# Kernel tuning notes

Measured on AMD Instinct MI355X. Metric: run time of the kernel, lower is better.

Reference implementation:

```python
import jax, jax.numpy as jnp
import numpy as np

N_NODES = 100000
N_EDGES = 1600000


def _sage_layer(x, src, dst, Wl, bl, Wr):
    # PyG SAGEConv (aggr='mean', root_weight=True):
    #   out_i = lin_l(mean_{j in N(i)} x_j) + lin_r(x_i)
    msg = x[src]                                              # [E, d] gather
    summed = jax.ops.segment_sum(msg, dst, num_segments=N_NODES)
    cnt = jax.ops.segment_sum(jnp.ones((src.shape[0],), x.dtype), dst,
                              num_segments=N_NODES)
    mean = summed / jnp.maximum(cnt, 1.0)[:, None]            # zero-deg nodes -> 0
    return mean @ Wl + bl + x @ Wr


def setup_inputs() -> dict:
    key = jax.random.key(0)
    ks = jax.random.split(key, 12)
    d_in, d_h, d_out = 6, 128, 64

    def lin(k, fi, fo):
        s = 1.0 / np.sqrt(fi)
        return jax.random.uniform(k, (fi, fo), jnp.float32, -s, s)

    return {
        "x": jax.random.normal(ks[0], (N_NODES, 10), jnp.float32),
        "edge_index": jax.random.randint(ks[1], (2, N_EDGES), 0, N_NODES),
        "Wl0": lin(ks[2], d_in, d_h), "bl0": jnp.zeros((d_h,), jnp.float32),
        "Wr0": lin(ks[3], d_in, d_h),
        "Wl1": lin(ks[4], d_h, d_h), "bl1": jnp.zeros((d_h,), jnp.float32),
        "Wr1": lin(ks[5], d_h, d_h),
        "Wl2": lin(ks[6], d_h, d_out), "bl2": jnp.zeros((d_out,), jnp.float32),
        "Wr2": lin(ks[7], d_h, d_out),
    }


def reference(x, edge_index, Wl0, bl0, Wr0, Wl1, bl1, Wr1, Wl2, bl2, Wr2):
    src, dst = edge_index[0], edge_index[1]
    h = x[:, 4:10]                                            # bus feature slice
    h = jax.nn.relu(_sage_layer(h, src, dst, Wl0, bl0, Wr0))
    h = jax.nn.relu(_sage_layer(h, src, dst, Wl1, bl1, Wr1))
    h = jax.nn.relu(_sage_layer(h, src, dst, Wl2, bl2, Wr2))
    return h
```

## Files before the change

### kernel.cpp

```cpp
#include <hip/hip_runtime.h>


typedef __attribute__((ext_vector_type(8))) short bf16x8;
typedef __attribute__((ext_vector_type(4))) float f32x4;
typedef __attribute__((ext_vector_type(2))) float f32x2;

constexpr int PB = 256;
constexpr float F8SCALE = 32.0f;

static __device__ __forceinline__ int imax(int a, int b) { return a > b ? a : b; }

static __device__ __forceinline__ float bfbits_lo(unsigned u) {
    union { unsigned i; float f; } v; v.i = u << 16; return v.f;
}
static __device__ __forceinline__ float bfbits_hi(unsigned u) {
    union { unsigned i; float f; } v; v.i = u & 0xffff0000u; return v.f;
}
static __device__ __forceinline__ unsigned short f2bf(float f) {
    unsigned u = __float_as_uint(f);
    u = (u + 0x7fffu + ((u >> 16) & 1u)) >> 16;
    return (unsigned short)u;
}
static __device__ __forceinline__ unsigned pack2bf(float a, float b) {
    return (unsigned)f2bf(a) | ((unsigned)f2bf(b) << 16);
}
static __device__ __forceinline__ void acc_f8x4(unsigned u, float* a) {
    f32x2 lo = __builtin_amdgcn_cvt_pk_f32_fp8((int)u, false);
    f32x2 hi = __builtin_amdgcn_cvt_pk_f32_fp8((int)u, true);
    a[0] += lo[0]; a[1] += lo[1]; a[2] += hi[0]; a[3] += hi[1];
}
static __device__ __forceinline__ void acc_bf8(uint4 v, float* a) {
    a[0] += bfbits_lo(v.x); a[1] += bfbits_hi(v.x);
    a[2] += bfbits_lo(v.y); a[3] += bfbits_hi(v.y);
    a[4] += bfbits_lo(v.z); a[5] += bfbits_hi(v.z);
    a[6] += bfbits_lo(v.w); a[7] += bfbits_hi(v.w);
}


__global__ __launch_bounds__(256) void k_p1count(const int* __restrict__ dst,
                                                 int* __restrict__ C,
                                                 int nE, int nbk, int epb) {
    __shared__ int h[512];
    for (int i = threadIdx.x; i < nbk; i += 256) h[i] = 0;
    __syncthreads();
    int e0 = blockIdx.x * epb;
    int e1 = min(e0 + epb, nE);
    for (int i = e0 + threadIdx.x; i < e1; i += 256)
        atomicAdd(&h[dst[i] >> 8], 1);
    __syncthreads();
    for (int i = threadIdx.x; i < nbk; i += 256)
        C[blockIdx.x * nbk + i] = h[i];
}

__global__ __launch_bounds__(256) void k_colscan(int* __restrict__ C,
                                                 int* __restrict__ tot, int nbk) {
    __shared__ int sm[256];
    int k = blockIdx.x, t = threadIdx.x;
    int v = C[t * nbk + k];
    sm[t] = v;
    __syncthreads();
    for (int o = 1; o < 256; o <<= 1) {
        int u = (t >= o) ? sm[t - o] : 0;
        __syncthreads();
        sm[t] += u;
        __syncthreads();
    }
    C[t * nbk + k] = sm[t] - v;
    if (t == 255) tot[k] = sm[255];
}

__global__ __launch_bounds__(256) void k_scan_a(const int* __restrict__ cnt,
                                                int* __restrict__ offs, int n) {
    __shared__ int sm[256];
    int t = threadIdx.x;
    int base = t * 4;
    int v0 = 0, v1 = 0, v2 = 0, v3 = 0;
    if (base + 3 < n) {
        int4 q = *(const int4*)(cnt + base);
        v0 = q.x; v1 = q.y; v2 = q.z; v3 = q.w;
    } else {
        if (base < n)     v0 = cnt[base];
        if (base + 1 < n) v1 = cnt[base + 1];
        if (base + 2 < n) v2 = cnt[base + 2];
    }
    int s = v0 + v1 + v2 + v3;
    sm[t] = s;
    __syncthreads();
    for (int o = 1; o < 256; o <<= 1) {
        int u = (t >= o) ? sm[t - o] : 0;
        __syncthreads();
        sm[t] += u;
        __syncthreads();
    }
    int excl = sm[t] - s;
    if (base < n)     offs[base]     = excl;
    if (base + 1 < n) offs[base + 1] = excl + v0;
    if (base + 2 < n) offs[base + 2] = excl + v0 + v1;
    if (base + 3 < n) offs[base + 3] = excl + v0 + v1 + v2;
    if (t == 255) offs[n] = sm[255];
}

__global__ __launch_bounds__(256) void k_p1fill(const int* __restrict__ src,
                                                const int* __restrict__ dst,
                                                const int* __restrict__ bstart,
                                                const int* __restrict__ C,
                                                unsigned* __restrict__ ebuf,
                                                int nE, int nbk, int epb) {
    __shared__ int cur[512];
    int b = blockIdx.x;
    for (int i = threadIdx.x; i < nbk; i += 256)
        cur[i] = bstart[i] + C[b * nbk + i];
    __syncthreads();
    int e0 = b * epb;
    int e1 = min(e0 + epb, nE);
    for (int i = e0 + threadIdx.x; i < e1; i += 256) {
        int d = dst[i];
        unsigned s = (unsigned)src[i];
        int p = atomicAdd(&cur[d >> 8], 1);
        ebuf[p] = (s << 8) | (unsigned)(d & 255);
    }
}

__global__ __launch_bounds__(256) void k_p2fill(const unsigned* __restrict__ ebuf,
                                                const int* __restrict__ bstart,
                                                int* __restrict__ offs,
                                                int* __restrict__ csr,
                                                int nN, int nE) {
    __shared__ int h[256], sm[256], cur[256];
    int k = blockIdx.x, t = threadIdx.x;
    int base = bstart[k], end = bstart[k + 1];
    h[t] = 0;
    __syncthreads();
    for (int i = base + t; i < end; i += 256)
        atomicAdd(&h[ebuf[i] & 255u], 1);
    __syncthreads();
    int v = h[t];
    sm[t] = v;
    __syncthreads();
    for (int o = 1; o < 256; o <<= 1) {
        int u = (t >= o) ? sm[t - o] : 0;
        __syncthreads();
        sm[t] += u;
        __syncthreads();
    }
    int excl = sm[t] - v;
    int node = (k << 8) + t;
    if (node < nN) offs[node] = base + excl;
    cur[t] = base + excl;
    if (k == 0 && t == 0) offs[nN] = nE;
    __syncthreads();
    for (int i = base + t; i < end; i += 256) {
        unsigned e = ebuf[i];
        int p = atomicAdd(&cur[e & 255u], 1);
        csr[p] = (int)(e >> 8);
    }
}


static __device__ __forceinline__ void wtfrag_one(const float* __restrict__ W1,
                                                  const float* __restrict__ W2,
                                                  unsigned short* __restrict__ Wt,
                                                  int K1, int K, int N, int c) {
    int NB = N >> 4;
    int lane = c & 63;
    int n = (c >> 6) % NB;
    int ks = c / (NB << 6);
    int row = n * 16 + (lane & 15);
    int col = ks * 32 + (lane >> 4) * 8;
    unsigned short o[8];
#pragma unroll
    for (int j = 0; j < 8; ++j) {
        int k = col + j;
        float v = (k < K1) ? W1[k * N + row] : W2[(k - K1) * N + row];
        o[j] = f2bf(v);
    }
    *(uint4*)(Wt + (size_t)c * 8) = *(const uint4*)o;
}

__global__ __launch_bounds__(256) void k_wtfrag_all(const float* __restrict__ Wl1,
                                                    const float* __restrict__ Wr1,
                                                    const float* __restrict__ Wl2,
                                                    const float* __restrict__ Wr2,
                                                    unsigned short* __restrict__ Wt1,
                                                    unsigned short* __restrict__ Wt2l,
                                                    unsigned short* __restrict__ Wt2r) {
    int c = blockIdx.x * 256 + threadIdx.x;
    if (c < 4096)      wtfrag_one(Wl1, Wr1, Wt1, 128, 256, 128, c);
    else if (c < 5120) wtfrag_one(Wl2, Wl2, Wt2l, 128, 128, 64, c - 4096);
    else if (c < 6144) wtfrag_one(Wr2, Wr2, Wt2r, 128, 128, 64, c - 5120);
}


__global__ __launch_bounds__(256) void k_agg0(const float* __restrict__ x,
                                              const int* __restrict__ offs,
                                              const int* __restrict__ csr,
                                              float* __restrict__ mean0, int nN) {
    int i = blockIdx.x * blockDim.x + threadIdx.x;
    if (i >= nN) return;
    int lo = offs[i], hi = offs[i + 1];
    float a0 = 0, a1 = 0, a2 = 0, a3 = 0, a4 = 0, a5 = 0;
    int e = lo;
    for (; e + 4 <= hi; e += 4) {
        int s0 = csr[e], s1 = csr[e + 1], s2 = csr[e + 2], s3 = csr[e + 3];
        const float* r0 = x + (size_t)s0 * 10 + 4;
        const float* r1 = x + (size_t)s1 * 10 + 4;
        const float* r2 = x + (size_t)s2 * 10 + 4;
        const float* r3 = x + (size_t)s3 * 10 + 4;
        float2 u0 = *(const float2*)(r0), u1 = *(const float2*)(r0 + 2), u2 = *(const float2*)(r0 + 4);
        float2 w0 = *(const float2*)(r1), w1 = *(const float2*)(r1 + 2), w2 = *(const float2*)(r1 + 4);
        float2 p0 = *(const float2*)(r2), p1 = *(const float2*)(r2 + 2), p2 = *(const float2*)(r2 + 4);
        float2 q0 = *(const float2*)(r3), q1 = *(const float2*)(r3 + 2), q2 = *(const float2*)(r3 + 4);
        a0 += u0.x + w0.x + p0.x + q0.x;
        a1 += u0.y + w0.y + p0.y + q0.y;
        a2 += u1.x + w1.x + p1.x + q1.x;
        a3 += u1.y + w1.y + p1.y + q1.y;
        a4 += u2.x + w2.x + p2.x + q2.x;
        a5 += u2.y + w2.y + p2.y + q2.y;
    }
    for (; e < hi; ++e) {
        int s = csr[e];
        const float* r = x + (size_t)s * 10 + 4;
        float2 v0 = *(const float2*)(r);
        float2 v1 = *(const float2*)(r + 2);
        float2 v2 = *(const float2*)(r + 4);
        a0 += v0.x; a1 += v0.y; a2 += v1.x; a3 += v1.y; a4 += v2.x; a5 += v2.y;
    }
    float inv = 1.0f / (float)imax(hi - lo, 1);
    float* o = mean0 + (size_t)i * 6;
    o[0] = a0 * inv; o[1] = a1 * inv; o[2] = a2 * inv;
    o[3] = a3 * inv; o[4] = a4 * inv; o[5] = a5 * inv;
}

__global__ __launch_bounds__(256) void k_agg128f8(const unsigned char* __restrict__ X,
                                                  const int* __restrict__ offs,
                                                  const int* __restrict__ csr,
                                                  unsigned short* __restrict__ M, int nN) {
    int idx = blockIdx.x * 256 + threadIdx.x;
    int node = idx >> 3;
    int fl = idx & 7;
    if (node >= nN) return;
    int lo = offs[node], hi = offs[node + 1];
    float a[16];
#pragma unroll
    for (int j = 0; j < 16; ++j) a[j] = 0.f;
    int e = lo;
    for (; e + 8 <= hi; e += 8) {
        uint4 v0 = *(const uint4*)(X + (size_t)csr[e + 0] * 128 + fl * 16);
        uint4 v1 = *(const uint4*)(X + (size_t)csr[e + 1] * 128 + fl * 16);
        uint4 v2 = *(const uint4*)(X + (size_t)csr[e + 2] * 128 + fl * 16);
        uint4 v3 = *(const uint4*)(X + (size_t)csr[e + 3] * 128 + fl * 16);
        uint4 v4 = *(const uint4*)(X + (size_t)csr[e + 4] * 128 + fl * 16);
        uint4 v5 = *(const uint4*)(X + (size_t)csr[e + 5] * 128 + fl * 16);
        uint4 v6 = *(const uint4*)(X + (size_t)csr[e + 6] * 128 + fl * 16);
        uint4 v7 = *(const uint4*)(X + (size_t)csr[e + 7] * 128 + fl * 16);
        acc_f8x4(v0.x, a + 0); acc_f8x4(v0.y, a + 4); acc_f8x4(v0.z, a + 8); acc_f8x4(v0.w, a + 12);
        acc_f8x4(v1.x, a + 0); acc_f8x4(v1.y, a + 4); acc_f8x4(v1.z, a + 8); acc_f8x4(v1.w, a + 12);
        acc_f8x4(v2.x, a + 0); acc_f8x4(v2.y, a + 4); acc_f8x4(v2.z, a + 8); acc_f8x4(v2.w, a + 12);
        acc_f8x4(v3.x, a + 0); acc_f8x4(v3.y, a + 4); acc_f8x4(v3.z, a + 8); acc_f8x4(v3.w, a + 12);
        acc_f8x4(v4.x, a + 0); acc_f8x4(v4.y, a + 4); acc_f8x4(v4.z, a + 8); acc_f8x4(v4.w, a + 12);
        acc_f8x4(v5.x, a + 0); acc_f8x4(v5.y, a + 4); acc_f8x4(v5.z, a + 8); acc_f8x4(v5.w, a + 12);
        acc_f8x4(v6.x, a + 0); acc_f8x4(v6.y, a + 4); acc_f8x4(v6.z, a + 8); acc_f8x4(v6.w, a + 12);
        acc_f8x4(v7.x, a + 0); acc_f8x4(v7.y, a + 4); acc_f8x4(v7.z, a + 8); acc_f8x4(v7.w, a + 12);
    }
    for (; e + 4 <= hi; e += 4) {
        uint4 v0 = *(const uint4*)(X + (size_t)csr[e + 0] * 128 + fl * 16);
        uint4 v1 = *(const uint4*)(X + (size_t)csr[e + 1] * 128 + fl * 16);
        uint4 v2 = *(const uint4*)(X + (size_t)csr[e + 2] * 128 + fl * 16);
        uint4 v3 = *(const uint4*)(X + (size_t)csr[e + 3] * 128 + fl * 16);
        acc_f8x4(v0.x, a + 0); acc_f8x4(v0.y, a + 4); acc_f8x4(v0.z, a + 8); acc_f8x4(v0.w, a + 12);
        acc_f8x4(v1.x, a + 0); acc_f8x4(v1.y, a + 4); acc_f8x4(v1.z, a + 8); acc_f8x4(v1.w, a + 12);
        acc_f8x4(v2.x, a + 0); acc_f8x4(v2.y, a + 4); acc_f8x4(v2.z, a + 8); acc_f8x4(v2.w, a + 12);
        acc_f8x4(v3.x, a + 0); acc_f8x4(v3.y, a + 4); acc_f8x4(v3.z, a + 8); acc_f8x4(v3.w, a + 12);
    }
    for (; e < hi; ++e) {
        uint4 v = *(const uint4*)(X + (size_t)csr[e] * 128 + fl * 16);
        acc_f8x4(v.x, a + 0); acc_f8x4(v.y, a + 4); acc_f8x4(v.z, a + 8); acc_f8x4(v.w, a + 12);
    }
    float inv = 1.0f / (F8SCALE * (float)imax(hi - lo, 1));
    unsigned o[8];
#pragma unroll
    for (int j = 0; j < 8; ++j) o[j] = pack2bf(a[2 * j] * inv, a[2 * j + 1] * inv);
    unsigned short* mp = M + (size_t)node * 128 + fl * 16;
    *(uint4*)(mp)     = *(const uint4*)(o);
    *(uint4*)(mp + 8) = *(const uint4*)(o + 4);
}

__global__ __launch_bounds__(256) void k_agg64(const unsigned short* __restrict__ X,
                                               const int* __restrict__ offs,
                                               const int* __restrict__ csr,
                                               float* __restrict__ M, int nN) {
    int idx = blockIdx.x * 256 + threadIdx.x;
    int node = idx >> 3;
    int fl = idx & 7;
    if (node >= nN) return;
    int lo = offs[node], hi = offs[node + 1];
    float a[8] = {0, 0, 0, 0, 0, 0, 0, 0};
    int e = lo;
    for (; e + 8 <= hi; e += 8) {
        uint4 v0 = *(const uint4*)(X + (size_t)csr[e + 0] * 64 + fl * 8);
        uint4 v1 = *(const uint4*)(X + (size_t)csr[e + 1] * 64 + fl * 8);
        uint4 v2 = *(const uint4*)(X + (size_t)csr[e + 2] * 64 + fl * 8);
        uint4 v3 = *(const uint4*)(X + (size_t)csr[e + 3] * 64 + fl * 8);
        uint4 v4 = *(const uint4*)(X + (size_t)csr[e + 4] * 64 + fl * 8);
        uint4 v5 = *(const uint4*)(X + (size_t)csr[e + 5] * 64 + fl * 8);
        uint4 v6 = *(const uint4*)(X + (size_t)csr[e + 6] * 64 + fl * 8);
        uint4 v7 = *(const uint4*)(X + (size_t)csr[e + 7] * 64 + fl * 8);
        acc_bf8(v0, a); acc_bf8(v1, a); acc_bf8(v2, a); acc_bf8(v3, a);
        acc_bf8(v4, a); acc_bf8(v5, a); acc_bf8(v6, a); acc_bf8(v7, a);
    }
    for (; e + 4 <= hi; e += 4) {
        uint4 v0 = *(const uint4*)(X + (size_t)csr[e + 0] * 64 + fl * 8);
        uint4 v1 = *(const uint4*)(X + (size_t)csr[e + 1] * 64 + fl * 8);
        uint4 v2 = *(const uint4*)(X + (size_t)csr[e + 2] * 64 + fl * 8);
        uint4 v3 = *(const uint4*)(X + (size_t)csr[e + 3] * 64 + fl * 8);
        acc_bf8(v0, a); acc_bf8(v1, a); acc_bf8(v2, a); acc_bf8(v3, a);
    }
    for (; e < hi; ++e) {
        uint4 v = *(const uint4*)(X + (size_t)csr[e] * 64 + fl * 8);
        acc_bf8(v, a);
    }
    float inv = 1.0f / (float)imax(hi - lo, 1);
    float* o = M + (size_t)node * 64 + fl * 8;
    *(float4*)(o)     = make_float4(a[0] * inv, a[1] * inv, a[2] * inv, a[3] * inv);
    *(float4*)(o + 4) = make_float4(a[4] * inv, a[5] * inv, a[6] * inv, a[7] * inv);
}


__global__ __launch_bounds__(256) void k_l0(const float* __restrict__ x,
                                            const float* __restrict__ mean0,
                                            const float* __restrict__ Wl,
                                            const float* __restrict__ bl,
                                            const float* __restrict__ Wr,
                                            unsigned short* __restrict__ out,
                                            unsigned char* __restrict__ out8, int nN) {
    int idx = blockIdx.x * 256 + threadIdx.x;
    int node = idx >> 4;
    int j0 = (idx & 15) * 8;
    if (node >= nN) return;
    const float* mp = mean0 + (size_t)node * 6;
    float2 m01 = *(const float2*)mp, m23 = *(const float2*)(mp + 2), m45 = *(const float2*)(mp + 4);
    const float* hp = x + (size_t)node * 10 + 4;
    float2 h01 = *(const float2*)hp, h23 = *(const float2*)(hp + 2), h45 = *(const float2*)(hp + 4);
    float m[6] = {m01.x, m01.y, m23.x, m23.y, m45.x, m45.y};
    float h[6] = {h01.x, h01.y, h23.x, h23.y, h45.x, h45.y};
    float4 b0 = *(const float4*)(bl + j0);
    float4 b1 = *(const float4*)(bl + j0 + 4);
    float v[8] = {b0.x, b0.y, b0.z, b0.w, b1.x, b1.y, b1.z, b1.w};
#pragma unroll
    for (int k = 0; k < 6; ++k) {
        float4 w0 = *(const float4*)(Wl + k * 128 + j0);
        float4 w1 = *(const float4*)(Wl + k * 128 + j0 + 4);
        v[0] = fmaf(m[k], w0.x, v[0]); v[1] = fmaf(m[k], w0.y, v[1]);
        v[2] = fmaf(m[k], w0.z, v[2]); v[3] = fmaf(m[k], w0.w, v[3]);
        v[4] = fmaf(m[k], w1.x, v[4]); v[5] = fmaf(m[k], w1.y, v[5]);
        v[6] = fmaf(m[k], w1.z, v[6]); v[7] = fmaf(m[k], w1.w, v[7]);
    }
#pragma unroll
    for (int k = 0; k < 6; ++k) {
        float4 w0 = *(const float4*)(Wr + k * 128 + j0);
        float4 w1 = *(const float4*)(Wr + k * 128 + j0 + 4);
        v[0] = fmaf(h[k], w0.x, v[0]); v[1] = fmaf(h[k], w0.y, v[1]);
        v[2] = fmaf(h[k], w0.z, v[2]); v[3] = fmaf(h[k], w0.w, v[3]);
        v[4] = fmaf(h[k], w1.x, v[4]); v[5] = fmaf(h[k], w1.y, v[5]);
        v[6] = fmaf(h[k], w1.z, v[6]); v[7] = fmaf(h[k], w1.w, v[7]);
    }
#pragma unroll
    for (int t = 0; t < 8; ++t) v[t] = fmaxf(v[t], 0.f);
    unsigned ob[4];
#pragma unroll
    for (int t = 0; t < 4; ++t) ob[t] = pack2bf(v[2 * t], v[2 * t + 1]);
    *(uint4*)(out + (size_t)node * 128 + j0) = *(const uint4*)ob;
    int d0 = __builtin_amdgcn_cvt_pk_fp8_f32(v[0] * F8SCALE, v[1] * F8SCALE, 0, false);
    d0     = __builtin_amdgcn_cvt_pk_fp8_f32(v[2] * F8SCALE, v[3] * F8SCALE, d0, true);
    int d1 = __builtin_amdgcn_cvt_pk_fp8_f32(v[4] * F8SCALE, v[5] * F8SCALE, 0, false);
    d1     = __builtin_amdgcn_cvt_pk_fp8_f32(v[6] * F8SCALE, v[7] * F8SCALE, d1, true);
    uint2 o8; o8.x = (unsigned)d0; o8.y = (unsigned)d1;
    *(uint2*)(out8 + (size_t)node * 128 + j0) = o8;
}


template <int KA, int KB, int N, bool RELU, bool BF16OUT, bool HASBIAS, bool HASADD>
__global__ __launch_bounds__(256) void k_mfma(const unsigned short* __restrict__ A0,
                                              const unsigned short* __restrict__ A1,
                                              const unsigned short* __restrict__ Wt,
                                              const float* __restrict__ bias,
                                              const float* __restrict__ add,
                                              void* __restrict__ Cout, int nN) {
    constexpr int K = KA + KB;
    constexpr int NSTEP = K / 32;
    constexpr int NB = N / 16;
    const int tid = threadIdx.x;
    const int wave = (blockIdx.x * 256 + tid) >> 6;
    const int m0 = wave * 32;
    if (m0 >= nN) return;
    const int lane = tid & 63;
    const int lr = lane & 15;
    const int lk = lane >> 4;

    f32x4 acc[2][NB];
#pragma unroll
    for (int g = 0; g < 2; ++g)
#pragma unroll
        for (int n = 0; n < NB; ++n) acc[g][n] = (f32x4){0.f, 0.f, 0.f, 0.f};

    auto loadA = [&](int kk, bf16x8& a0, bf16x8& a1) {
        const unsigned short* Ap;
        int lda, krel;
        if (KB > 0 && kk >= KA) { Ap = A1; lda = KB; krel = kk - KA; }
        else                    { Ap = A0; lda = KA; krel = kk; }
        a0 = *(const bf16x8*)(Ap + (size_t)(m0 + lr) * lda + krel + lk * 8);
        a1 = *(const bf16x8*)(Ap + (size_t)(m0 + 16 + lr) * lda + krel + lk * 8);
    };
    auto loadB = [&](int ks, bf16x8* b) {
        const unsigned short* Wk = Wt + (((size_t)ks * NB) << 6) * 8 + lane * 8;
#pragma unroll
        for (int n = 0; n < NB; ++n)
            b[n] = *(const bf16x8*)(Wk + ((size_t)n << 6) * 8);
    };

    bf16x8 a0c, a1c, a0n, a1n;
    bf16x8 bc[NB], bn[NB];
    loadA(0, a0c, a1c);
    loadB(0, bc);

#pragma unroll
    for (int ks = 0; ks < NSTEP; ++ks) {
        if (ks + 1 < NSTEP) {
            loadA((ks + 1) * 32, a0n, a1n);
            loadB(ks + 1, bn);
        }
#pragma unroll
        for (int n = 0; n < NB; ++n) {
            acc[0][n] = __builtin_amdgcn_mfma_f32_16x16x32_bf16(a0c, bc[n], acc[0][n], 0, 0, 0);
            acc[1][n] = __builtin_amdgcn_mfma_f32_16x16x32_bf16(a1c, bc[n], acc[1][n], 0, 0, 0);
        }
        if (ks + 1 < NSTEP) {
            a0c = a0n; a1c = a1n;
#pragma unroll
            for (int n = 0; n < NB; ++n) bc[n] = bn[n];
        }
    }

#pragma unroll
    for (int g = 0; g < 2; ++g) {
#pragma unroll
        for (int r = 0; r < 4; ++r) {
            int gm = m0 + g * 16 + lk * 4 + r;
#pragma unroll
            for (int n = 0; n < NB; ++n) {
                float v = acc[g][n][r];
                if (HASBIAS) v += bias[n * 16 + lr];
                if (HASADD)  v += add[(size_t)gm * N + n * 16 + lr];
                if (RELU)    v = fmaxf(v, 0.f);
                if (BF16OUT) ((unsigned short*)Cout)[(size_t)gm * N + n * 16 + lr] = f2bf(v);
                else         ((float*)Cout)[(size_t)gm * N + n * 16 + lr] = v;
            }
        }
    }
}


extern "C" void kernel_launch(void* const* d_in, const int* in_sizes, int n_in,
                              void* d_out, int out_size, void* d_ws, size_t ws_size,
                              hipStream_t stream) {
    const float* x   = (const float*)d_in[0];
    const int*   ei  = (const int*)d_in[1];
    const float* Wl0 = (const float*)d_in[2];
    const float* bl0 = (const float*)d_in[3];
    const float* Wr0 = (const float*)d_in[4];
    const float* Wl1 = (const float*)d_in[5];
    const float* bl1 = (const float*)d_in[6];
    const float* Wr1 = (const float*)d_in[7];
    const float* Wl2 = (const float*)d_in[8];
    const float* bl2 = (const float*)d_in[9];
    const float* Wr2 = (const float*)d_in[10];

    const int nN = in_sizes[0] / 10;
    const int nE = in_sizes[1] / 2;
    const int* src = ei;
    const int* dst = ei + nE;
    const int nbk = (nN + 255) >> 8;
    const int epb = (nE + PB - 1) / PB;

    char* ws = (char*)d_ws;
    size_t off = 0;
    auto alloc = [&](size_t bytes) -> char* {
        char* p = ws + off;
        off = (off + bytes + 255) & ~(size_t)255;
        return p;
    };
    unsigned short* out0   = (unsigned short*)alloc((size_t)nN * 128 * 2);
    unsigned char*  out0f8 = (unsigned char*)alloc((size_t)nN * 128);
    unsigned short* mean1  = (unsigned short*)alloc((size_t)nN * 128 * 2);
    unsigned short* out1   = (unsigned short*)alloc((size_t)nN * 128 * 2);
    float* mean0 = (float*)alloc((size_t)nN * 6 * 4);
    unsigned short* Wt1  = (unsigned short*)alloc((size_t)128 * 256 * 2);
    unsigned short* Wt2l = (unsigned short*)alloc((size_t)64 * 128 * 2);
    unsigned short* Wt2r = (unsigned short*)alloc((size_t)64 * 128 * 2);
    int* C      = (int*)alloc((size_t)PB * nbk * 4);
    int* tot    = (int*)alloc((size_t)nbk * 4);
    int* bstart = (int*)alloc(((size_t)nbk + 1) * 4);
    int* offs   = (int*)alloc(((size_t)nN + 1) * 4);
    int* csr    = (int*)alloc((size_t)nE * 4);
    unsigned* ebuf = (unsigned*)alloc((size_t)nE * 4);

    unsigned short* z2     = out0;
    float*          meanz2 = (float*)mean1;

    k_wtfrag_all<<<24, 256, 0, stream>>>(Wl1, Wr1, Wl2, Wr2, Wt1, Wt2l, Wt2r);

    k_p1count<<<PB, 256, 0, stream>>>(dst, C, nE, nbk, epb);
    k_colscan<<<nbk, 256, 0, stream>>>(C, tot, nbk);
    k_scan_a<<<1, 256, 0, stream>>>(tot, bstart, nbk);
    k_p1fill<<<PB, 256, 0, stream>>>(src, dst, bstart, C, ebuf, nE, nbk, epb);
    k_p2fill<<<nbk, 256, 0, stream>>>(ebuf, bstart, offs, csr, nN, nE);

    k_agg0<<<(nN + 255) / 256, 256, 0, stream>>>(x, offs, csr, mean0, nN);
    k_l0<<<((size_t)nN * 16 + 255) / 256, 256, 0, stream>>>(x, mean0, Wl0, bl0, Wr0, out0, out0f8, nN);

    const int gemm_grid = (nN / 32 + 3) / 4 + 1;

    k_agg128f8<<<((size_t)nN * 8 + 255) / 256, 256, 0, stream>>>(out0f8, offs, csr, mean1, nN);
    k_mfma<128, 128, 128, true, true, true, false><<<gemm_grid, 256, 0, stream>>>(
        mean1, out0, Wt1, bl1, nullptr, out1, nN);

    k_mfma<128, 0, 64, false, true, false, false><<<gemm_grid, 256, 0, stream>>>(
        out1, nullptr, Wt2l, nullptr, nullptr, z2, nN);
    k_agg64<<<((size_t)nN * 8 + 255) / 256, 256, 0, stream>>>(z2, offs, csr, meanz2, nN);
    k_mfma<128, 0, 64, true, false, true, true><<<gemm_grid, 256, 0, stream>>>(
        out1, nullptr, Wt2r, bl2, meanz2, (float*)d_out, nN);
}
```

Before: 221.0 us.

## Fuse layer-0 aggregation with linear, merge layer-2 GEMMs, fold epilogue into aggregation

The layer-0 mean aggregation and its linear layer become one kernel, with 16 lanes per node cooperatively gathering neighbors and reducing through shuffles. Layer 2's two GEMMs (Wl2 and Wr2) are merged into a single 128-wide MFMA pass that writes z2 as bf16 and y2 as fp32. The final bias, add and relu move into the 64-wide aggregation kernel. Weight prep is fused into the edge-count kernel. Together these cut several launches and the mean0/meanz2 round trips through memory, at the cost of more shuffles and an extra fp32 y2 buffer.

```diff
diff --git a/kernel.cpp b/kernel.cpp
--- a/kernel.cpp
+++ b/kernel.cpp
@@ -6,6 +6,7 @@
 typedef __attribute__((ext_vector_type(2))) float f32x2;
 
 constexpr int PB = 256;
+constexpr int WTCH = 6144;
 constexpr float F8SCALE = 32.0f;
 
 static __device__ __forceinline__ int imax(int a, int b) { return a > b ? a : b; }
@@ -37,20 +38,75 @@
 }
 
 
-__global__ __launch_bounds__(256) void k_p1count(const int* __restrict__ dst,
-                                                 int* __restrict__ C,
-                                                 int nE, int nbk, int epb) {
+static __device__ __forceinline__ void wtfrag_katk(const float* __restrict__ W1,
+                                                   const float* __restrict__ W2,
+                                                   unsigned short* __restrict__ Wt,
+                                                   int K1, int K, int N, int c) {
+    int NB = N >> 4;
+    int lane = c & 63;
+    int n = (c >> 6) % NB;
+    int ks = c / (NB << 6);
+    int row = n * 16 + (lane & 15);
+    int col = ks * 32 + (lane >> 4) * 8;
+    unsigned short o[8];
+#pragma unroll
+    for (int j = 0; j < 8; ++j) {
+        int k = col + j;
+        float v = (k < K1) ? W1[k * N + row] : W2[(k - K1) * N + row];
+        o[j] = f2bf(v);
+    }
+    *(uint4*)(Wt + (size_t)c * 8) = *(const uint4*)o;
+}
+
+static __device__ __forceinline__ void wtfrag_natn(const float* __restrict__ Wa,
+                                                   const float* __restrict__ Wb,
+                                                   unsigned short* __restrict__ Wt,
+                                                   int K, int Nh, int c) {
+    int NB = (2 * Nh) >> 4;
+    int lane = c & 63;
+    int n = (c >> 6) % NB;
+    int ks = c / (NB << 6);
+    int row = n * 16 + (lane & 15);
+    int col = ks * 32 + (lane >> 4) * 8;
+    unsigned short o[8];
+#pragma unroll
+    for (int j = 0; j < 8; ++j) {
+        int k = col + j;
+        float v = (row < Nh) ? Wa[k * Nh + row] : Wb[k * Nh + (row - Nh)];
+        o[j] = f2bf(v);
+    }
+    *(uint4*)(Wt + (size_t)c * 8) = *(const uint4*)o;
+}
+
+
+__global__ __launch_bounds__(256) void k_prep(const float* __restrict__ Wl1,
+                                              const float* __restrict__ Wr1,
+                                              const float* __restrict__ Wl2,
+                                              const float* __restrict__ Wr2,
+                                              unsigned short* __restrict__ Wt1,
+                                              unsigned short* __restrict__ Wt2,
+                                              const int* __restrict__ dst,
+                                              int* __restrict__ C,
+                                              int nE, int nbk, int epb) {
+    if (blockIdx.x < 24) {
+        int c = blockIdx.x * 256 + threadIdx.x;
+        if (c < 4096)        wtfrag_katk(Wl1, Wr1, Wt1, 128, 256, 128, c);
+        else if (c < WTCH)   wtfrag_natn(Wl2, Wr2, Wt2, 128, 64, c - 4096);
+        return;
+    }
     __shared__ int h[512];
+    int b = blockIdx.x - 24;
     for (int i = threadIdx.x; i < nbk; i += 256) h[i] = 0;
     __syncthreads();
-    int e0 = blockIdx.x * epb;
+    int e0 = b * epb;
     int e1 = min(e0 + epb, nE);
     for (int i = e0 + threadIdx.x; i < e1; i += 256)
         atomicAdd(&h[dst[i] >> 8], 1);
     __syncthreads();
     for (int i = threadIdx.x; i < nbk; i += 256)
-        C[blockIdx.x * nbk + i] = h[i];
-}
+        C[b * nbk + i] = h[i];
+}
+
 
 __global__ __launch_bounds__(256) void k_colscan(int* __restrict__ C,
                                                  int* __restrict__ tot, int nbk) {
@@ -157,67 +213,21 @@
 }
 
 
-static __device__ __forceinline__ void wtfrag_one(const float* __restrict__ W1,
-                                                  const float* __restrict__ W2,
-                                                  unsigned short* __restrict__ Wt,
-                                                  int K1, int K, int N, int c) {
-    int NB = N >> 4;
-    int lane = c & 63;
-    int n = (c >> 6) % NB;
-    int ks = c / (NB << 6);
-    int row = n * 16 + (lane & 15);
-    int col = ks * 32 + (lane >> 4) * 8;
-    unsigned short o[8];
-#pragma unroll
-    for (int j = 0; j < 8; ++j) {
-        int k = col + j;
-        float v = (k < K1) ? W1[k * N + row] : W2[(k - K1) * N + row];
-        o[j] = f2bf(v);
-    }
-    *(uint4*)(Wt + (size_t)c * 8) = *(const uint4*)o;
-}
-
-__global__ __launch_bounds__(256) void k_wtfrag_all(const float* __restrict__ Wl1,
-                                                    const float* __restrict__ Wr1,
-                                                    const float* __restrict__ Wl2,
-                                                    const float* __restrict__ Wr2,
-                                                    unsigned short* __restrict__ Wt1,
-                                                    unsigned short* __restrict__ Wt2l,
-                                                    unsigned short* __restrict__ Wt2r) {
-    int c = blockIdx.x * 256 + threadIdx.x;
-    if (c < 4096)      wtfrag_one(Wl1, Wr1, Wt1, 128, 256, 128, c);
-    else if (c < 5120) wtfrag_one(Wl2, Wl2, Wt2l, 128, 128, 64, c - 4096);
-    else if (c < 6144) wtfrag_one(Wr2, Wr2, Wt2r, 128, 128, 64, c - 5120);
-}
-
-
-__global__ __launch_bounds__(256) void k_agg0(const float* __restrict__ x,
-                                              const int* __restrict__ offs,
-                                              const int* __restrict__ csr,
-                                              float* __restrict__ mean0, int nN) {
-    int i = blockIdx.x * blockDim.x + threadIdx.x;
-    if (i >= nN) return;
-    int lo = offs[i], hi = offs[i + 1];
+__global__ __launch_bounds__(256) void k_l0f(const float* __restrict__ x,
+                                             const int* __restrict__ offs,
+                                             const int* __restrict__ csr,
+                                             const float* __restrict__ Wl,
+                                             const float* __restrict__ bl,
+                                             const float* __restrict__ Wr,
+                                             unsigned short* __restrict__ out,
+                                             unsigned char* __restrict__ out8, int nN) {
+    int idx = blockIdx.x * 256 + threadIdx.x;
+    int node = idx >> 4;
+    int j = threadIdx.x & 15;
+    if (node >= nN) return;
+    int lo = offs[node], hi = offs[node + 1];
     float a0 = 0, a1 = 0, a2 = 0, a3 = 0, a4 = 0, a5 = 0;
-    int e = lo;
-    for (; e + 4 <= hi; e += 4) {
-        int s0 = csr[e], s1 = csr[e + 1], s2 = csr[e + 2], s3 = csr[e + 3];
-        const float* r0 = x + (size_t)s0 * 10 + 4;
-        const float* r1 = x + (size_t)s1 * 10 + 4;
-        const float* r2 = x + (size_t)s2 * 10 + 4;
-        const float* r3 = x + (size_t)s3 * 10 + 4;
-        float2 u0 = *(const float2*)(r0), u1 = *(const float2*)(r0 + 2), u2 = *(const float2*)(r0 + 4);
-        float2 w0 = *(const float2*)(r1), w1 = *(const float2*)(r1 + 2), w2 = *(const float2*)(r1 + 4);
-        float2 p0 = *(const float2*)(r2), p1 = *(const float2*)(r2 + 2), p2 = *(const float2*)(r2 + 4);
-        float2 q0 = *(const float2*)(r3), q1 = *(const float2*)(r3 + 2), q2 = *(const float2*)(r3 + 4);
-        a0 += u0.x + w0.x + p0.x + q0.x;
-        a1 += u0.y + w0.y + p0.y + q0.y;
-        a2 += u1.x + w1.x + p1.x + q1.x;
-        a3 += u1.y + w1.y + p1.y + q1.y;
-        a4 += u2.x + w2.x + p2.x + q2.x;
-        a5 += u2.y + w2.y + p2.y + q2.y;
-    }
-    for (; e < hi; ++e) {
+    for (int e = lo + j; e < hi; e += 16) {
         int s = csr[e];
         const float* r = x + (size_t)s * 10 + 4;
         float2 v0 = *(const float2*)(r);
@@ -225,11 +235,53 @@
         float2 v2 = *(const float2*)(r + 4);
         a0 += v0.x; a1 += v0.y; a2 += v1.x; a3 += v1.y; a4 += v2.x; a5 += v2.y;
     }
+#pragma unroll
+    for (int mask = 1; mask < 16; mask <<= 1) {
+        a0 += __shfl_xor(a0, mask); a1 += __shfl_xor(a1, mask);
+        a2 += __shfl_xor(a2, mask); a3 += __shfl_xor(a3, mask);
+        a4 += __shfl_xor(a4, mask); a5 += __shfl_xor(a5, mask);
+    }
     float inv = 1.0f / (float)imax(hi - lo, 1);
-    float* o = mean0 + (size_t)i * 6;
-    o[0] = a0 * inv; o[1] = a1 * inv; o[2] = a2 * inv;
-    o[3] = a3 * inv; o[4] = a4 * inv; o[5] = a5 * inv;
-}
+    float m[6] = {a0 * inv, a1 * inv, a2 * inv, a3 * inv, a4 * inv, a5 * inv};
+    const float* hp = x + (size_t)node * 10 + 4;
+    float2 h01 = *(const float2*)hp, h23 = *(const float2*)(hp + 2), h45 = *(const float2*)(hp + 4);
+    float h[6] = {h01.x, h01.y, h23.x, h23.y, h45.x, h45.y};
+    int j0 = j * 8;
+    float4 b0 = *(const float4*)(bl + j0);
+    float4 b1 = *(const float4*)(bl + j0 + 4);
+    float v[8] = {b0.x, b0.y, b0.z, b0.w, b1.x, b1.y, b1.z, b1.w};
+#pragma unroll
+    for (int k = 0; k < 6; ++k) {
+        float4 w0 = *(const float4*)(Wl + k * 128 + j0);
+        float4 w1 = *(const float4*)(Wl + k * 128 + j0 + 4);
+        v[0] = fmaf(m[k], w0.x, v[0]); v[1] = fmaf(m[k], w0.y, v[1]);
+        v[2] = fmaf(m[k], w0.z, v[2]); v[3] = fmaf(m[k], w0.w, v[3]);
+        v[4] = fmaf(m[k], w1.x, v[4]); v[5] = fmaf(m[k], w1.y, v[5]);
+        v[6] = fmaf(m[k], w1.z, v[6]); v[7] = fmaf(m[k], w1.w, v[7]);
+    }
+#pragma unroll
+    for (int k = 0; k < 6; ++k) {
+        float4 w0 = *(const float4*)(Wr + k * 128 + j0);
+        float4 w1 = *(const float4*)(Wr + k * 128 + j0 + 4);
+        v[0] = fmaf(h[k], w0.x, v[0]); v[1] = fmaf(h[k], w0.y, v[1]);
+        v[2] = fmaf(h[k], w0.z, v[2]); v[3] = fmaf(h[k], w0.w, v[3]);
+        v[4] = fmaf(h[k], w1.x, v[4]); v[5] = fmaf(h[k], w1.y, v[5]);
+        v[6] = fmaf(h[k], w1.z, v[6]); v[7] = fmaf(h[k], w1.w, v[7]);
+    }
+#pragma unroll
+    for (int t = 0; t < 8; ++t) v[t] = fmaxf(v[t], 0.f);
+    unsigned ob[4];
+#pragma unroll
+    for (int t = 0; t < 4; ++t) ob[t] = pack2bf(v[2 * t], v[2 * t + 1]);
+    *(uint4*)(out + (size_t)node * 128 + j0) = *(const uint4*)ob;
+    int d0 = __builtin_amdgcn_cvt_pk_fp8_f32(v[0] * F8SCALE, v[1] * F8SCALE, 0, false);
+    d0     = __builtin_amdgcn_cvt_pk_fp8_f32(v[2] * F8SCALE, v[3] * F8SCALE, d0, true);
+    int d1 = __builtin_amdgcn_cvt_pk_fp8_f32(v[4] * F8SCALE, v[5] * F8SCALE, 0, false);
+    d1     = __builtin_amdgcn_cvt_pk_fp8_f32(v[6] * F8SCALE, v[7] * F8SCALE, d1, true);
+    uint2 o8; o8.x = (unsigned)d0; o8.y = (unsigned)d1;
+    *(uint2*)(out8 + (size_t)node * 128 + j0) = o8;
+}
+
 
 __global__ __launch_bounds__(256) void k_agg128f8(const unsigned char* __restrict__ X,
                                                   const int* __restrict__ offs,
@@ -285,10 +337,12 @@
     *(uint4*)(mp + 8) = *(const uint4*)(o + 4);
 }
 
-__global__ __launch_bounds__(256) void k_agg64(const unsigned short* __restrict__ X,
-                                               const int* __restrict__ offs,
-                                               const int* __restrict__ csr,
-                                               float* __restrict__ M, int nN) {
+__global__ __launch_bounds__(256) void k_agg64f(const unsigned short* __restrict__ X,
+                                                const int* __restrict__ offs,
+                                                const int* __restrict__ csr,
+                                                const float* __restrict__ y2,
+                                                const float* __restrict__ bl2,
+                                                float* __restrict__ out, int nN) {
     int idx = blockIdx.x * 256 + threadIdx.x;
     int node = idx >> 3;
     int fl = idx & 7;
@@ -320,72 +374,29 @@
         acc_bf8(v, a);
     }
     float inv = 1.0f / (float)imax(hi - lo, 1);
-    float* o = M + (size_t)node * 64 + fl * 8;
-    *(float4*)(o)     = make_float4(a[0] * inv, a[1] * inv, a[2] * inv, a[3] * inv);
-    *(float4*)(o + 4) = make_float4(a[4] * inv, a[5] * inv, a[6] * inv, a[7] * inv);
-}
-
-
-__global__ __launch_bounds__(256) void k_l0(const float* __restrict__ x,
-                                            const float* __restrict__ mean0,
-                                            const float* __restrict__ Wl,
-                                            const float* __restrict__ bl,
-                                            const float* __restrict__ Wr,
-                                            unsigned short* __restrict__ out,
-                                            unsigned char* __restrict__ out8, int nN) {
-    int idx = blockIdx.x * 256 + threadIdx.x;
-    int node = idx >> 4;
-    int j0 = (idx & 15) * 8;
-    if (node >= nN) return;
-    const float* mp = mean0 + (size_t)node * 6;
-    float2 m01 = *(const float2*)mp, m23 = *(const float2*)(mp + 2), m45 = *(const float2*)(mp + 4);
-    const float* hp = x + (size_t)node * 10 + 4;
-    float2 h01 = *(const float2*)hp, h23 = *(const float2*)(hp + 2), h45 = *(const float2*)(hp + 4);
-    float m[6] = {m01.x, m01.y, m23.x, m23.y, m45.x, m45.y};
-    float h[6] = {h01.x, h01.y, h23.x, h23.y, h45.x, h45.y};
-    float4 b0 = *(const float4*)(bl + j0);
-    float4 b1 = *(const float4*)(bl + j0 + 4);
-    float v[8] = {b0.x, b0.y, b0.z, b0.w, b1.x, b1.y, b1.z, b1.w};
-#pragma unroll
-    for (int k = 0; k < 6; ++k) {
-        float4 w0 = *(const float4*)(Wl + k * 128 + j0);
-        float4 w1 = *(const float4*)(Wl + k * 128 + j0 + 4);
-        v[0] = fmaf(m[k], w0.x, v[0]); v[1] = fmaf(m[k], w0.y, v[1]);
-        v[2] = fmaf(m[k], w0.z, v[2]); v[3] = fmaf(m[k], w0.w, v[3]);
-        v[4] = fmaf(m[k], w1.x, v[4]); v[5] = fmaf(m[k], w1.y, v[5]);
-        v[6] = fmaf(m[k], w1.z, v[6]); v[7] = fmaf(m[k], w1.w, v[7]);
-    }
-#pragma unroll
-    for (int k = 0; k < 6; ++k) {
-        float4 w0 = *(const float4*)(Wr + k * 128 + j0);
-        float4 w1 = *(const float4*)(Wr + k * 128 + j0 + 4);
-        v[0] = fmaf(h[k], w0.x, v[0]); v[1] = fmaf(h[k], w0.y, v[1]);
-        v[2] = fmaf(h[k], w0.z, v[2]); v[3] = fmaf(h[k], w0.w, v[3]);
-        v[4] = fmaf(h[k], w1.x, v[4]); v[5] = fmaf(h[k], w1.y, v[5]);
-        v[6] = fmaf(h[k], w1.z, v[6]); v[7] = fmaf(h[k], w1.w, v[7]);
-    }
-#pragma unroll
-    for (int t = 0; t < 8; ++t) v[t] = fmaxf(v[t], 0.f);
-    unsigned ob[4];
-#pragma unroll
-    for (int t = 0; t < 4; ++t) ob[t] = pack2bf(v[2 * t], v[2 * t + 1]);
-    *(uint4*)(out + (size_t)node * 128 + j0) = *(const uint4*)ob;
-    int d0 = __builtin_amdgcn_cvt_pk_fp8_f32(v[0] * F8SCALE, v[1] * F8SCALE, 0, false);
-    d0     = __builtin_amdgcn_cvt_pk_fp8_f32(v[2] * F8SCALE, v[3] * F8SCALE, d0, true);
-    int d1 = __builtin_amdgcn_cvt_pk_fp8_f32(v[4] * F8SCALE, v[5] * F8SCALE, 0, false);
-    d1     = __builtin_amdgcn_cvt_pk_fp8_f32(v[6] * F8SCALE, v[7] * F8SCALE, d1, true);
-    uint2 o8; o8.x = (unsigned)d0; o8.y = (unsigned)d1;
-    *(uint2*)(out8 + (size_t)node * 128 + j0) = o8;
-}
-
-
-template <int KA, int KB, int N, bool RELU, bool BF16OUT, bool HASBIAS, bool HASADD>
+    const float* yp = y2 + (size_t)node * 64 + fl * 8;
+    float4 ya = *(const float4*)yp;
+    float4 yb = *(const float4*)(yp + 4);
+    float4 ba = *(const float4*)(bl2 + fl * 8);
+    float4 bb = *(const float4*)(bl2 + fl * 8 + 4);
+    float* o = out + (size_t)node * 64 + fl * 8;
+    *(float4*)(o) = make_float4(fmaxf(fmaf(a[0], inv, ya.x + ba.x), 0.f),
+                                fmaxf(fmaf(a[1], inv, ya.y + ba.y), 0.f),
+                                fmaxf(fmaf(a[2], inv, ya.z + ba.z), 0.f),
+                                fmaxf(fmaf(a[3], inv, ya.w + ba.w), 0.f));
+    *(float4*)(o + 4) = make_float4(fmaxf(fmaf(a[4], inv, yb.x + bb.x), 0.f),
+                                    fmaxf(fmaf(a[5], inv, yb.y + bb.y), 0.f),
+                                    fmaxf(fmaf(a[6], inv, yb.z + bb.z), 0.f),
+                                    fmaxf(fmaf(a[7], inv, yb.w + bb.w), 0.f));
+}
+
+
+template <int KA, int KB, int N>
 __global__ __launch_bounds__(256) void k_mfma(const unsigned short* __restrict__ A0,
                                               const unsigned short* __restrict__ A1,
                                               const unsigned short* __restrict__ Wt,
                                               const float* __restrict__ bias,
-                                              const float* __restrict__ add,
-                                              void* __restrict__ Cout, int nN) {
+                                              unsigned short* __restrict__ Cout, int nN) {
     constexpr int K = KA + KB;
     constexpr int NSTEP = K / 32;
     constexpr int NB = N / 16;
@@ -448,13 +459,78 @@
             int gm = m0 + g * 16 + lk * 4 + r;
 #pragma unroll
             for (int n = 0; n < NB; ++n) {
-                float v = acc[g][n][r];
-                if (HASBIAS) v += bias[n * 16 + lr];
-                if (HASADD)  v += add[(size_t)gm * N + n * 16 + lr];
-                if (RELU)    v = fmaxf(v, 0.f);
-                if (BF16OUT) ((unsigned short*)Cout)[(size_t)gm * N + n * 16 + lr] = f2bf(v);
-                else         ((float*)Cout)[(size_t)gm * N + n * 16 + lr] = v;
+                float v = fmaxf(acc[g][n][r] + bias[n * 16 + lr], 0.f);
+                Cout[(size_t)gm * N + n * 16 + lr] = f2bf(v);
             }
+        }
+    }
+}
+
+
+__global__ __launch_bounds__(256) void k_mfma_l2(const unsigned short* __restrict__ A0,
+                                                 const unsigned short* __restrict__ Wt,
+                                                 unsigned short* __restrict__ z2,
+                                                 float* __restrict__ y2, int nN) {
+    constexpr int K = 128, NSTEP = 4, NB = 8;
+    const int tid = threadIdx.x;
+    const int wave = (blockIdx.x * 256 + tid) >> 6;
+    const int m0 = wave * 32;
+    if (m0 >= nN) return;
+    const int lane = tid & 63;
+    const int lr = lane & 15;
+    const int lk = lane >> 4;
+
+    f32x4 acc[2][NB];
+#pragma unroll
+    for (int g = 0; g < 2; ++g)
+#pragma unroll
+        for (int n = 0; n < NB; ++n) acc[g][n] = (f32x4){0.f, 0.f, 0.f, 0.f};
+
+    auto loadA = [&](int kk, bf16x8& a0, bf16x8& a1) {
+        a0 = *(const bf16x8*)(A0 + (size_t)(m0 + lr) * K + kk + lk * 8);
+        a1 = *(const bf16x8*)(A0 + (size_t)(m0 + 16 + lr) * K + kk + lk * 8);
+    };
+    auto loadB = [&](int ks, bf16x8* b) {
+        const unsigned short* Wk = Wt + (((size_t)ks * NB) << 6) * 8 + lane * 8;
+#pragma unroll
+        for (int n = 0; n < NB; ++n)
+            b[n] = *(const bf16x8*)(Wk + ((size_t)n << 6) * 8);
+    };
+
+    bf16x8 a0c, a1c, a0n, a1n;
+    bf16x8 bc[NB], bn[NB];
+    loadA(0, a0c, a1c);
+    loadB(0, bc);
+
+#pragma unroll
+    for (int ks = 0; ks < NSTEP; ++ks) {
+        if (ks + 1 < NSTEP) {
+            loadA((ks + 1) * 32, a0n, a1n);
+            loadB(ks + 1, bn);
+        }
+#pragma unroll
+        for (int n = 0; n < NB; ++n) {
+            acc[0][n] = __builtin_amdgcn_mfma_f32_16x16x32_bf16(a0c, bc[n], acc[0][n], 0, 0, 0);
+            acc[1][n] = __builtin_amdgcn_mfma_f32_16x16x32_bf16(a1c, bc[n], acc[1][n], 0, 0, 0);
+        }
+        if (ks + 1 < NSTEP) {
+            a0c = a0n; a1c = a1n;
+#pragma unroll
+            for (int n = 0; n < NB; ++n) bc[n] = bn[n];
+        }
+    }
+
+#pragma unroll
+    for (int g = 0; g < 2; ++g) {
+#pragma unroll
+        for (int r = 0; r < 4; ++r) {
+            int gm = m0 + g * 16 + lk * 4 + r;
+#pragma unroll
+            for (int n = 0; n < 4; ++n)
+                z2[(size_t)gm * 64 + n * 16 + lr] = f2bf(acc[g][n][r]);
+#pragma unroll
+            for (int n = 4; n < 8; ++n)
+                y2[(size_t)gm * 64 + (n - 4) * 16 + lr] = acc[g][n][r];
         }
     }
 }
@@ -493,10 +569,8 @@
     unsigned char*  out0f8 = (unsigned char*)alloc((size_t)nN * 128);
     unsigned short* mean1  = (unsigned short*)alloc((size_t)nN * 128 * 2);
     unsigned short* out1   = (unsigned short*)alloc((size_t)nN * 128 * 2);
-    float* mean0 = (float*)alloc((size_t)nN * 6 * 4);
-    unsigned short* Wt1  = (unsigned short*)alloc((size_t)128 * 256 * 2);
-    unsigned short* Wt2l = (unsigned short*)alloc((size_t)64 * 128 * 2);
-    unsigned short* Wt2r = (unsigned short*)alloc((size_t)64 * 128 * 2);
+    unsigned short* Wt1 = (unsigned short*)alloc((size_t)128 * 256 * 2);
+    unsigned short* Wt2 = (unsigned short*)alloc((size_t)128 * 128 * 2);
     int* C      = (int*)alloc((size_t)PB * nbk * 4);
     int* tot    = (int*)alloc((size_t)nbk * 4);
     int* bstart = (int*)alloc(((size_t)nbk + 1) * 4);
@@ -504,29 +578,24 @@
     int* csr    = (int*)alloc((size_t)nE * 4);
     unsigned* ebuf = (unsigned*)alloc((size_t)nE * 4);
 
-    unsigned short* z2     = out0;
-    float*          meanz2 = (float*)mean1;
-
-    k_wtfrag_all<<<24, 256, 0, stream>>>(Wl1, Wr1, Wl2, Wr2, Wt1, Wt2l, Wt2r);
-
-    k_p1count<<<PB, 256, 0, stream>>>(dst, C, nE, nbk, epb);
+    unsigned short* z2 = out0;
+    float*          y2 = (float*)mean1;
+
+    k_prep<<<24 + PB, 256, 0, stream>>>(Wl1, Wr1, Wl2, Wr2, Wt1, Wt2, dst, C, nE, nbk, epb);
     k_colscan<<<nbk, 256, 0, stream>>>(C, tot, nbk);
     k_scan_a<<<1, 256, 0, stream>>>(tot, bstart, nbk);
     k_p1fill<<<PB, 256, 0, stream>>>(src, dst, bstart, C, ebuf, nE, nbk, epb);
     k_p2fill<<<nbk, 256, 0, stream>>>(ebuf, bstart, offs, csr, nN, nE);
 
-    k_agg0<<<(nN + 255) / 256, 256, 0, stream>>>(x, offs, csr, mean0, nN);
-    k_l0<<<((size_t)nN * 16 + 255) / 256, 256, 0, stream>>>(x, mean0, Wl0, bl0, Wr0, out0, out0f8, nN);
+    k_l0f<<<((size_t)nN * 16 + 255) / 256, 256, 0, stream>>>(
+        x, offs, csr, Wl0, bl0, Wr0, out0, out0f8, nN);
 
     const int gemm_grid = (nN / 32 + 3) / 4 + 1;
 
     k_agg128f8<<<((size_t)nN * 8 + 255) / 256, 256, 0, stream>>>(out0f8, offs, csr, mean1, nN);
-    k_mfma<128, 128, 128, true, true, true, false><<<gemm_grid, 256, 0, stream>>>(
-        mean1, out0, Wt1, bl1, nullptr, out1, nN);
-
-    k_mfma<128, 0, 64, false, true, false, false><<<gemm_grid, 256, 0, stream>>>(
-        out1, nullptr, Wt2l, nullptr, nullptr, z2, nN);
-    k_agg64<<<((size_t)nN * 8 + 255) / 256, 256, 0, stream>>>(z2, offs, csr, meanz2, nN);
-    k_mfma<128, 0, 64, true, false, true, true><<<gemm_grid, 256, 0, stream>>>(
-        out1, nullptr, Wt2r, bl2, meanz2, (float*)d_out, nN);
-}
+    k_mfma<128, 128, 128><<<gemm_grid, 256, 0, stream>>>(mean1, out0, Wt1, bl1, out1, nN);
+
+    k_mfma_l2<<<gemm_grid, 256, 0, stream>>>(out1, Wt2, z2, y2, nN);
+    k_agg64f<<<((size_t)nN * 8 + 255) / 256, 256, 0, stream>>>(
+        z2, offs, csr, y2, bl2, (float*)d_out, nN);
+}
```

After: 198.8 us, median of 2. 1.11x faster.
